# Kernel optimization log

Hardware: AMD Instinct MI355X
Metric: run time of the kernel (lower is better)

## Reference

```python
import jax, jax.numpy as jnp
import numpy as np

B, N = 2, 16384
GRID = (256, 256, 32)
LOWER = jnp.array([-51.2, -51.2, -3.2], jnp.float32)
UPPER = jnp.array([51.2, 51.2, 3.2], jnp.float32)
VOX = 0.4  # uniform voxel size (required by the SPC assertion in the original)
FREE = 17
MIN_DIST = 2.5
EVAL_LOWER = LOWER
EVAL_UPPER = UPPER
MAX_DIST = float(np.linalg.norm(np.array([102.4, 102.4, 6.4])))  # norm(upper - lower)
EPS = 1e-9


def setup_inputs() -> dict:
    key = jax.random.key(0)
    k_occ, k_sel, k_pts = jax.random.split(key, 3)
    labels = jax.random.randint(k_occ, (B,) + GRID, 0, 17, dtype=jnp.int32)
    sel = jax.random.uniform(k_sel, (B,) + GRID) < 0.05
    occupancy = jnp.where(sel, labels, FREE).astype(jnp.int32)
    # lidar points in sensor frame, xy in [-50, 50], z in [-3, 3]
    u = jax.random.uniform(k_pts, (B, N, 3), dtype=jnp.float32)
    points_lidar = u * jnp.array([100.0, 100.0, 6.0]) + jnp.array([-50.0, -50.0, -3.0])
    points_mask = jnp.ones((B, N), dtype=bool)
    T = jnp.eye(4, dtype=jnp.float32).at[:3, 3].set(jnp.array([0.8, 0.3, 1.7]))
    ego_from_lidar = jnp.broadcast_to(T, (B, 4, 4))
    return {
        "occupancy": occupancy,
        "points_lidar": points_lidar,
        "points_mask": points_mask,
        "ego_from_lidar": ego_from_lidar,
    }


def _apply_tf(T, p):
    # T: [B,4,4] homogeneous, p: [B,N,3]
    return jnp.einsum('bij,bnj->bni', T[:, :3, :3], p) + T[:, None, :3, 3]


def _traverse(occupancy, start_v, dirn, ray_len):
    """Exact voxel-grid ray traversal (replaces kaolin SPC unbatched_raytrace).

    start_v, dirn: [B,N,3] in voxel coordinates; ray_len: [B,N] in voxel units.
    Returns (first_hit_t [B,N] in voxel units, num_transmissions [B,N]).
    """
    Gx, Gy, Gz = GRID
    planes = jnp.concatenate([
        jnp.arange(Gx + 1), jnp.arange(Gy + 1), jnp.arange(Gz + 1)
    ]).astype(jnp.float32)  # [K]
    axid = jnp.concatenate([
        jnp.zeros(Gx + 1, jnp.int32), jnp.ones(Gy + 1, jnp.int32),
        jnp.full(Gz + 1, 2, jnp.int32)
    ])  # [K]
    s_ax = start_v[..., axid]          # [B,N,K]
    d_ax = dirn[..., axid]             # [B,N,K]
    t = jnp.where(jnp.abs(d_ax) > EPS, (planes - s_ax) / d_ax, jnp.inf)
    t = jnp.where(t >= 0.0, t, jnp.inf)          # only forward crossings
    b, n = start_v.shape[:2]
    t = jnp.concatenate([jnp.zeros((b, n, 1), t.dtype), t], axis=-1)  # start voxel at t=0
    t = jnp.sort(t, axis=-1)
    entry = t[..., :-1]
    tm = 0.5 * (entry + t[..., 1:])               # segment midpoints -> voxel ids
    vx = jnp.floor(start_v[..., 0][..., None] + tm * dirn[..., 0][..., None]).astype(jnp.int32)
    vy = jnp.floor(start_v[..., 1][..., None] + tm * dirn[..., 1][..., None]).astype(jnp.int32)
    vz = jnp.floor(start_v[..., 2][..., None] + tm * dirn[..., 2][..., None]).astype(jnp.int32)
    inb = ((vx >= 0) & (vx < Gx) & (vy >= 0) & (vy < Gy) & (vz >= 0) & (vz < Gz)
           & jnp.isfinite(tm))
    lin = (jnp.clip(vx, 0, Gx - 1) * Gy + jnp.clip(vy, 0, Gy - 1)) * Gz + jnp.clip(vz, 0, Gz - 1)
    occ_flat = occupancy.reshape(b, -1)
    k = lin.shape[-1]
    lbl = jax.vmap(jnp.take)(occ_flat, lin.reshape(b, -1)).reshape(b, n, k)
    occ_hit = inb & (lbl != FREE)
    first_t = jnp.min(jnp.where(occ_hit, entry, jnp.inf), axis=-1)
    ntrans = jnp.sum((occ_hit & (entry < ray_len[..., None])).astype(jnp.float32), axis=-1)
    return first_t, ntrans


def reference(occupancy, points_lidar, points_mask, ego_from_lidar):
    start_ego = jnp.broadcast_to(ego_from_lidar[:, None, :3, 3], points_lidar.shape)
    end_ego = _apply_tf(ego_from_lidar, points_lidar)
    # to voxel coordinates
    start_v = (start_ego - LOWER) / VOX
    end_v = (end_ego - LOWER) / VOX
    ray = end_v - start_v
    ray_len = jnp.linalg.norm(ray, axis=-1)
    dirn = ray / ray_len[..., None]
    first_t, ntrans = _traverse(occupancy, start_v, dirn, ray_len)
    depth = first_t * VOX  # back to metric units (scale)
    lidar_depth = jnp.linalg.norm(points_lidar, axis=-1)
    rendered = jnp.where(points_mask, depth, jnp.nan)
    ntrans = jnp.where(points_mask, ntrans, jnp.nan)
    finite_depth = jnp.isfinite(rendered) & points_mask & (lidar_depth > MIN_DIST)
    rendered = jnp.minimum(rendered, MAX_DIST)  # clamp_max (inf -> MAX_DIST)
    d_ego = end_ego - start_ego
    dn_ego = d_ego / jnp.linalg.norm(d_ego, axis=-1, keepdims=True)
    end_r = start_ego + dn_ego * rendered[..., None]
    # clamp_points_along_line into eval volume
    seg = end_r - start_ego
    t_ax = jnp.where(seg > 0, (EVAL_UPPER - start_ego) / seg,
                     jnp.where(seg < 0, (EVAL_LOWER - start_ego) / seg, jnp.inf))
    t_cl = jnp.clip(jnp.min(t_ax, axis=-1), 0.0, 1.0)
    end_c = start_ego + t_cl[..., None] * seg
    rendered = jnp.linalg.norm(end_c - start_ego, axis=-1)
    in_vol = (jnp.all(end_ego >= EVAL_LOWER, -1) & jnp.all(end_ego <= EVAL_UPPER, -1)
              & jnp.all(start_ego >= EVAL_LOWER, -1) & jnp.all(start_ego <= EVAL_UPPER, -1)
              & points_mask & (lidar_depth > MIN_DIST))
    return rendered, ntrans, lidar_depth, in_vol, finite_depth
```

## Files before the change

kernel.cpp:

```cpp
#include <hip/hip_runtime.h>
#include <math.h>

#define GXI 256
#define GYI 256
#define GZI 32
#define NVOX (GXI * GYI * GZI)
#define NWORDS (NVOX / 32)
#define KB 4
#define NSEG 16
#define LOG2SEG 4

__global__ __launch_bounds__(256) void build_bitmap_kernel(
    const int* __restrict__ occ, unsigned int* __restrict__ bits, int nvox_total)
{
    int v = blockIdx.x * blockDim.x + threadIdx.x;
    bool occupied = false;
    if (v < nvox_total) occupied = (occ[v] != 17);
    unsigned long long m = __ballot(occupied);
    if ((threadIdx.x & 63) == 0 && v < nvox_total) {
        *(unsigned long long*)&bits[v >> 5] = m;
    }
}

__global__ __launch_bounds__(256, 8) void render_lidar_kernel(
    const unsigned int* __restrict__ bits,
    const float* __restrict__ pts,
    const float* __restrict__ ego,
    float* __restrict__ out,
    int B, int N)
{
#pragma clang fp contract(off)
    const float LX = -51.2f, LY = -51.2f, LZ = -3.2f;
    const float UX =  51.2f, UY =  51.2f, UZ =  3.2f;
    const float VOX = 0.4f;
    const float EPS = 1e-9f;
    const float MIN_DIST = 2.5f;
    const float MAX_DIST = (float)144.95682129669906;
    const float INF = __builtin_inff();

    int tid = blockIdx.x * blockDim.x + threadIdx.x;
    int total = B * N;
    int idx = tid >> LOG2SEG;
    int seg = tid & (NSEG - 1);
    if (idx >= total) return;
    int b = idx / N;

    float svx, svy, svz, dx, dy, dz, ray_len;
    {
        const float* T = ego + (size_t)b * 16;
        float sx = T[3], sy = T[7], sz = T[11];
        const float* p = pts + (size_t)idx * 3;
        float px = p[0], py = p[1], pz = p[2];
        float ex = ((T[0]*px + T[1]*py) + T[2]*pz) + sx;
        float ey = ((T[4]*px + T[5]*py) + T[6]*pz) + sy;
        float ez = ((T[8]*px + T[9]*py) + T[10]*pz) + sz;

        svx = (sx - LX) / VOX; svy = (sy - LY) / VOX; svz = (sz - LZ) / VOX;
        float evx = (ex - LX) / VOX, evy = (ey - LY) / VOX, evz = (ez - LZ) / VOX;
        float rx = evx - svx, ry = evy - svy, rz = evz - svz;
        ray_len = sqrtf((rx*rx + ry*ry) + rz*rz);
        dx = rx / ray_len; dy = ry / ray_len; dz = rz / ray_len;
    }

    float s3[3] = {svx, svy, svz};
    float d3[3] = {dx, dy, dz};
    const float G3[3] = {(float)GXI, (float)GYI, (float)GZI};

    float t_exit = INF;
    #pragma unroll
    for (int a = 0; a < 3; ++a) {
        float da = d3[a];
        if (fabsf(da) > EPS) {
            float bound = (da > 0.0f) ? G3[a] : 0.0f;
            float te = (bound - s3[a]) / da;
            if (te < t_exit) t_exit = te;
        }
    }

    float lo = t_exit * ((float)seg / (float)NSEG);
    float hi = (seg == NSEG - 1) ? INF : t_exit * ((float)(seg + 1) / (float)NSEG);

    float taA[3], tbA[3], pnA[3];
    float t_pred = 0.0f;
    #pragma unroll
    for (int a = 0; a < 3; ++a) {
        float da = d3[a], s = s3[a], G = G3[a];
        if (fabsf(da) > EPS) {
            float g, st;
            if (seg == 0) {
                if (da > 0.0f) { g = ceilf(s);  if (g < 0.0f) g = 0.0f; st = 1.0f; }
                else           { g = floorf(s); if (g > G)    g = G;    st = -1.0f; }
            } else if (da > 0.0f) {
                g = ceilf(s + lo * da); if (g < 0.0f) g = 0.0f;
                int it = 0;
                while (it < 8 && g <= G && (g - s) / da <= lo) { g += 1.0f; ++it; }
                it = 0;
                while (it < 8 && g >= 1.0f && ((g - 1.0f) - s) / da > lo) { g -= 1.0f; ++it; }
                st = 1.0f;
                float pp = g - 1.0f;
                if (pp >= 0.0f && pp <= G) {
                    float c = (pp - s) / da;
                    if (c >= 0.0f && c > t_pred) t_pred = c;
                }
            } else {
                g = floorf(s + lo * da); if (g > G) g = G;
                int it = 0;
                while (it < 8 && g >= 0.0f && (g - s) / da <= lo) { g -= 1.0f; ++it; }
                it = 0;
                while (it < 8 && g + 1.0f <= G && ((g + 1.0f) - s) / da > lo) { g += 1.0f; ++it; }
                st = -1.0f;
                float pp = g + 1.0f;
                if (pp >= 0.0f && pp <= G) {
                    float c = (pp - s) / da;
                    if (c >= 0.0f && c > t_pred) t_pred = c;
                }
            }
            taA[a] = (g >= 0.0f && g <= G) ? (g - s) / da : INF;
            float p1 = g + st;
            tbA[a] = (p1 >= 0.0f && p1 <= G) ? (p1 - s) / da : INF;
            pnA[a] = p1 + st;
        } else {
            taA[a] = INF; tbA[a] = INF; pnA[a] = 0.0f;
        }
    }
    float ta0 = taA[0], ta1 = taA[1], ta2 = taA[2];
    float tb0 = tbA[0], tb1 = tbA[1], tb2 = tbA[2];
    float pn0 = pnA[0], pn1 = pnA[1], pn2 = pnA[2];

    const unsigned int* bm = bits + (size_t)b * NWORDS;
    float t_cur = t_pred;
    float first_t = INF;
    float ntrans = 0.0f;
    bool was_in = false, have_hit = false, done = false;
    int guard = 0;

    while (true) {
        float tent[KB];
        int   linv[KB];
        int   vmask = 0;

        #pragma unroll
        for (int k = 0; k < KB; ++k) {
            tent[k] = 0.0f; linv[k] = 0;
            if (done) continue;
            float tn = fminf(fminf(ta0, ta1), ta2);
            if (tn == INF || tn > hi) { done = true; continue; }

            float tm = 0.5f * (t_cur + tn);
            int ix = (int)floorf(svx + tm * dx);
            int iy = (int)floorf(svy + tm * dy);
            int iz = (int)floorf(svz + tm * dz);
            bool inb = ((unsigned)ix < 256u) && ((unsigned)iy < 256u)
                    && ((unsigned)iz < 32u);

            bool a0 = (ta0 == tn);
            bool a1 = !a0 && (ta1 == tn);
            bool a2 = !(a0 || a1);
            float np = a0 ? pn0 : (a1 ? pn1 : pn2);
            float ss = a0 ? svx : (a1 ? svy : svz);
            float dd = a0 ? dx  : (a1 ? dy  : dz);
            float GG = a2 ? 32.0f : 256.0f;
            float st = (dd > 0.0f) ? 1.0f : -1.0f;
            float tnew = (np >= 0.0f && np <= GG) ? (np - ss) / dd : INF;
            ta0 = a0 ? tb0 : ta0;  tb0 = a0 ? tnew : tb0;  pn0 = a0 ? pn0 + st : pn0;
            ta1 = a1 ? tb1 : ta1;  tb1 = a1 ? tnew : tb1;  pn1 = a1 ? pn1 + st : pn1;
            ta2 = a2 ? tb2 : ta2;  tb2 = a2 ? tnew : tb2;  pn2 = a2 ? pn2 + st : pn2;

            if (inb) {
                was_in = true;
                tent[k] = t_cur;
                linv[k] = (ix << 13) + (iy << 5) + iz;
                vmask |= (1 << k);
            } else if (was_in) {
                done = true;
            }
            t_cur = tn;
        }

        unsigned int w[KB];
        #pragma unroll
        for (int k = 0; k < KB; ++k) w[k] = bm[linv[k] >> 5];

        #pragma unroll
        for (int k = 0; k < KB; ++k) {
            if ((vmask >> k) & 1) {
                if ((w[k] >> (linv[k] & 31)) & 1u) {
                    if (!have_hit) { first_t = tent[k]; have_hit = true; }
                    if (tent[k] < ray_len) ntrans += 1.0f;
                }
            }
        }

        if (done || (have_hit && t_cur >= ray_len)) break;
        if (++guard > 256) break;
    }

    float ft = first_t;
    float nt = ntrans;
    #pragma unroll
    for (int off = 1; off < NSEG; off <<= 1) {
        float ofv = __shfl_xor(ft, off);
        float onv = __shfl_xor(nt, off);
        ft = fminf(ft, ofv);
        nt += onv;
    }
    if (seg != 0) return;
    have_hit = (ft < INF);

    const float* T = ego + (size_t)b * 16;
    float sx = T[3], sy = T[7], sz = T[11];
    const float* p = pts + (size_t)idx * 3;
    float px = p[0], py = p[1], pz = p[2];
    float ex = ((T[0]*px + T[1]*py) + T[2]*pz) + sx;
    float ey = ((T[4]*px + T[5]*py) + T[6]*pz) + sy;
    float ez = ((T[8]*px + T[9]*py) + T[10]*pz) + sz;

    float depth = ft * VOX;
    float lidar_depth = sqrtf((px*px + py*py) + pz*pz);
    bool finite_depth = have_hit && (lidar_depth > MIN_DIST);
    float rendered = fminf(depth, MAX_DIST);

    float dgx = ex - sx, dgy = ey - sy, dgz = ez - sz;
    float dgn = sqrtf((dgx*dgx + dgy*dgy) + dgz*dgz);
    float dnx = dgx / dgn, dny = dgy / dgn, dnz = dgz / dgn;
    float erx = sx + dnx * rendered;
    float ery = sy + dny * rendered;
    float erz = sz + dnz * rendered;
    float sgx = erx - sx, sgy = ery - sy, sgz = erz - sz;
    float tax = sgx > 0.0f ? (UX - sx) / sgx : (sgx < 0.0f ? (LX - sx) / sgx : INF);
    float tay = sgy > 0.0f ? (UY - sy) / sgy : (sgy < 0.0f ? (LY - sy) / sgy : INF);
    float taz = sgz > 0.0f ? (UZ - sz) / sgz : (sgz < 0.0f ? (LZ - sz) / sgz : INF);
    float tmin = fminf(fminf(tax, tay), taz);
    float tcl = fminf(fmaxf(tmin, 0.0f), 1.0f);
    float ecx = sx + tcl * sgx;
    float ecy = sy + tcl * sgy;
    float ecz = sz + tcl * sgz;
    float ocx = ecx - sx, ocy = ecy - sy, ocz = ecz - sz;
    float rout = sqrtf((ocx*ocx + ocy*ocy) + ocz*ocz);

    bool in_vol = (ex >= LX) && (ex <= UX) && (ey >= LY) && (ey <= UY)
               && (ez >= LZ) && (ez <= UZ)
               && (sx >= LX) && (sx <= UX) && (sy >= LY) && (sy <= UY)
               && (sz >= LZ) && (sz <= UZ)
               && (lidar_depth > MIN_DIST);

    out[idx]             = rout;
    out[total + idx]     = nt;
    out[2 * total + idx] = lidar_depth;
    out[3 * total + idx] = in_vol ? 1.0f : 0.0f;
    out[4 * total + idx] = finite_depth ? 1.0f : 0.0f;
}

extern "C" void kernel_launch(void* const* d_in, const int* in_sizes, int n_in,
                              void* d_out, int out_size, void* d_ws, size_t ws_size,
                              hipStream_t stream) {
    const int*   occ = (const int*)d_in[0];
    const float* pts = (const float*)d_in[1];
    const float* ego = (const float*)d_in[3];

    int BN = in_sizes[2];
    int B  = in_sizes[3] / 16;
    int N  = BN / B;

    unsigned int* bits = (unsigned int*)d_ws;
    int nvox_total = B * NVOX;

    int pthreads = 256;
    int pblocks  = (nvox_total + pthreads - 1) / pthreads;
    build_bitmap_kernel<<<pblocks, pthreads, 0, stream>>>(occ, bits, nvox_total);

    int threads = 256;
    long long tthreads = (long long)BN * NSEG;
    int blocks = (int)((tthreads + threads - 1) / threads);
    render_lidar_kernel<<<blocks, threads, 0, stream>>>(bits, pts, ego, (float*)d_out, B, N);
}
```

Baseline: 40.05 us.

## Split ray segments over the in-range span and add a fallback pass for misses

The 16 cooperating lanes now split only the traversal span up to min(ray_len, grid exit) instead of the whole grid-exit span. A lane stops once it passes ray_len even if no hit has been found yet. A second cooperative pass walks the span from ray_len to grid exit, but only when no lane found a hit, and it stops at the first occupied voxel. This is meant to spread the ntrans-counting work more evenly across lanes and avoid walking the full ray every time, at the cost of extra code, divergence and a possible second traversal on rays that miss.

```diff
diff --git a/kernel.cpp b/kernel.cpp
--- a/kernel.cpp
+++ b/kernel.cpp
@@ -19,6 +19,51 @@
     unsigned long long m = __ballot(occupied);
     if ((threadIdx.x & 63) == 0 && v < nvox_total) {
         *(unsigned long long*)&bits[v >> 5] = m;
+    }
+}
+
+__device__ __forceinline__ void axis_init(
+    float s, float da, float G, float lo, bool seg0,
+    float& ta, float& tb, float& pn, float& tpred)
+{
+    const float EPS = 1e-9f;
+    const float INF = __builtin_inff();
+    if (fabsf(da) > EPS) {
+        float g, st;
+        if (seg0) {
+            if (da > 0.0f) { g = ceilf(s);  if (g < 0.0f) g = 0.0f; st = 1.0f; }
+            else           { g = floorf(s); if (g > G)    g = G;    st = -1.0f; }
+        } else if (da > 0.0f) {
+            g = ceilf(s + lo * da); if (g < 0.0f) g = 0.0f;
+            int it = 0;
+            while (it < 8 && g <= G && (g - s) / da <= lo) { g += 1.0f; ++it; }
+            it = 0;
+            while (it < 8 && g >= 1.0f && ((g - 1.0f) - s) / da > lo) { g -= 1.0f; ++it; }
+            st = 1.0f;
+            float pp = g - 1.0f;
+            if (pp >= 0.0f && pp <= G) {
+                float c = (pp - s) / da;
+                if (c >= 0.0f && c > tpred) tpred = c;
+            }
+        } else {
+            g = floorf(s + lo * da); if (g > G) g = G;
+            int it = 0;
+            while (it < 8 && g >= 0.0f && (g - s) / da <= lo) { g -= 1.0f; ++it; }
+            it = 0;
+            while (it < 8 && g + 1.0f <= G && ((g + 1.0f) - s) / da > lo) { g += 1.0f; ++it; }
+            st = -1.0f;
+            float pp = g + 1.0f;
+            if (pp >= 0.0f && pp <= G) {
+                float c = (pp - s) / da;
+                if (c >= 0.0f && c > tpred) tpred = c;
+            }
+        }
+        ta = (g >= 0.0f && g <= G) ? (g - s) / da : INF;
+        float p1 = g + st;
+        tb = (p1 >= 0.0f && p1 <= G) ? (p1 - s) / da : INF;
+        pn = p1 + st;
+    } else {
+        ta = INF; tb = INF; pn = 0.0f;
     }
 }
 
@@ -62,70 +107,23 @@
         dx = rx / ray_len; dy = ry / ray_len; dz = rz / ray_len;
     }
 
-    float s3[3] = {svx, svy, svz};
-    float d3[3] = {dx, dy, dz};
-    const float G3[3] = {(float)GXI, (float)GYI, (float)GZI};
-
     float t_exit = INF;
-    #pragma unroll
-    for (int a = 0; a < 3; ++a) {
-        float da = d3[a];
-        if (fabsf(da) > EPS) {
-            float bound = (da > 0.0f) ? G3[a] : 0.0f;
-            float te = (bound - s3[a]) / da;
-            if (te < t_exit) t_exit = te;
-        }
-    }
-
-    float lo = t_exit * ((float)seg / (float)NSEG);
-    float hi = (seg == NSEG - 1) ? INF : t_exit * ((float)(seg + 1) / (float)NSEG);
-
-    float taA[3], tbA[3], pnA[3];
+    {
+        if (fabsf(dx) > EPS) { float te = ((dx > 0.0f ? 256.0f : 0.0f) - svx) / dx; if (te < t_exit) t_exit = te; }
+        if (fabsf(dy) > EPS) { float te = ((dy > 0.0f ? 256.0f : 0.0f) - svy) / dy; if (te < t_exit) t_exit = te; }
+        if (fabsf(dz) > EPS) { float te = ((dz > 0.0f ?  32.0f : 0.0f) - svz) / dz; if (te < t_exit) t_exit = te; }
+    }
+    float RLc = fminf(ray_len, t_exit);
+
+    float lo = RLc * ((float)seg / (float)NSEG);
+    float hi = (seg == NSEG - 1) ? INF : RLc * ((float)(seg + 1) / (float)NSEG);
+
+    float ta0, tb0, pn0, ta1, tb1, pn1, ta2, tb2, pn2;
     float t_pred = 0.0f;
-    #pragma unroll
-    for (int a = 0; a < 3; ++a) {
-        float da = d3[a], s = s3[a], G = G3[a];
-        if (fabsf(da) > EPS) {
-            float g, st;
-            if (seg == 0) {
-                if (da > 0.0f) { g = ceilf(s);  if (g < 0.0f) g = 0.0f; st = 1.0f; }
-                else           { g = floorf(s); if (g > G)    g = G;    st = -1.0f; }
-            } else if (da > 0.0f) {
-                g = ceilf(s + lo * da); if (g < 0.0f) g = 0.0f;
-                int it = 0;
-                while (it < 8 && g <= G && (g - s) / da <= lo) { g += 1.0f; ++it; }
-                it = 0;
-                while (it < 8 && g >= 1.0f && ((g - 1.0f) - s) / da > lo) { g -= 1.0f; ++it; }
-                st = 1.0f;
-                float pp = g - 1.0f;
-                if (pp >= 0.0f && pp <= G) {
-                    float c = (pp - s) / da;
-                    if (c >= 0.0f && c > t_pred) t_pred = c;
-                }
-            } else {
-                g = floorf(s + lo * da); if (g > G) g = G;
-                int it = 0;
-                while (it < 8 && g >= 0.0f && (g - s) / da <= lo) { g -= 1.0f; ++it; }
-                it = 0;
-                while (it < 8 && g + 1.0f <= G && ((g + 1.0f) - s) / da > lo) { g += 1.0f; ++it; }
-                st = -1.0f;
-                float pp = g + 1.0f;
-                if (pp >= 0.0f && pp <= G) {
-                    float c = (pp - s) / da;
-                    if (c >= 0.0f && c > t_pred) t_pred = c;
-                }
-            }
-            taA[a] = (g >= 0.0f && g <= G) ? (g - s) / da : INF;
-            float p1 = g + st;
-            tbA[a] = (p1 >= 0.0f && p1 <= G) ? (p1 - s) / da : INF;
-            pnA[a] = p1 + st;
-        } else {
-            taA[a] = INF; tbA[a] = INF; pnA[a] = 0.0f;
-        }
-    }
-    float ta0 = taA[0], ta1 = taA[1], ta2 = taA[2];
-    float tb0 = tbA[0], tb1 = tbA[1], tb2 = tbA[2];
-    float pn0 = pnA[0], pn1 = pnA[1], pn2 = pnA[2];
+    bool s0 = (seg == 0);
+    axis_init(svx, dx, 256.0f, lo, s0, ta0, tb0, pn0, t_pred);
+    axis_init(svy, dy, 256.0f, lo, s0, ta1, tb1, pn1, t_pred);
+    axis_init(svz, dz,  32.0f, lo, s0, ta2, tb2, pn2, t_pred);
 
     const unsigned int* bm = bits + (size_t)b * NWORDS;
     float t_cur = t_pred;
@@ -191,7 +189,7 @@
             }
         }
 
-        if (done || (have_hit && t_cur >= ray_len)) break;
+        if (done || t_cur >= ray_len) break;
         if (++guard > 256) break;
     }
 
@@ -204,6 +202,88 @@
         ft = fminf(ft, ofv);
         nt += onv;
     }
+
+    if (ft == INF && t_exit > ray_len) {
+        float span = t_exit - ray_len;
+        float lo2 = ray_len + span * ((float)seg / (float)NSEG);
+        float hi2 = (seg == NSEG - 1) ? INF
+                  : ray_len + span * ((float)(seg + 1) / (float)NSEG);
+        float tp2 = 0.0f;
+        axis_init(svx, dx, 256.0f, lo2, false, ta0, tb0, pn0, tp2);
+        axis_init(svy, dy, 256.0f, lo2, false, ta1, tb1, pn1, tp2);
+        axis_init(svz, dz,  32.0f, lo2, false, ta2, tb2, pn2, tp2);
+        t_cur = tp2; was_in = false; done = false;
+        float ft2 = INF; bool hit2 = false;
+        guard = 0;
+
+        while (true) {
+            float tent[KB];
+            int   linv[KB];
+            int   vmask = 0;
+
+            #pragma unroll
+            for (int k = 0; k < KB; ++k) {
+                tent[k] = 0.0f; linv[k] = 0;
+                if (done) continue;
+                float tn = fminf(fminf(ta0, ta1), ta2);
+                if (tn == INF || tn > hi2) { done = true; continue; }
+
+                float tm = 0.5f * (t_cur + tn);
+                int ix = (int)floorf(svx + tm * dx);
+                int iy = (int)floorf(svy + tm * dy);
+                int iz = (int)floorf(svz + tm * dz);
+                bool inb = ((unsigned)ix < 256u) && ((unsigned)iy < 256u)
+                        && ((unsigned)iz < 32u);
+
+                bool a0 = (ta0 == tn);
+                bool a1 = !a0 && (ta1 == tn);
+                bool a2 = !(a0 || a1);
+                float np = a0 ? pn0 : (a1 ? pn1 : pn2);
+                float ss = a0 ? svx : (a1 ? svy : svz);
+                float dd = a0 ? dx  : (a1 ? dy  : dz);
+                float GG = a2 ? 32.0f : 256.0f;
+                float st = (dd > 0.0f) ? 1.0f : -1.0f;
+                float tnew = (np >= 0.0f && np <= GG) ? (np - ss) / dd : INF;
+                ta0 = a0 ? tb0 : ta0;  tb0 = a0 ? tnew : tb0;  pn0 = a0 ? pn0 + st : pn0;
+                ta1 = a1 ? tb1 : ta1;  tb1 = a1 ? tnew : tb1;  pn1 = a1 ? pn1 + st : pn1;
+                ta2 = a2 ? tb2 : ta2;  tb2 = a2 ? tnew : tb2;  pn2 = a2 ? pn2 + st : pn2;
+
+                if (inb) {
+                    was_in = true;
+                    tent[k] = t_cur;
+                    linv[k] = (ix << 13) + (iy << 5) + iz;
+                    vmask |= (1 << k);
+                } else if (was_in) {
+                    done = true;
+                }
+                t_cur = tn;
+            }
+
+            unsigned int w[KB];
+            #pragma unroll
+            for (int k = 0; k < KB; ++k) w[k] = bm[linv[k] >> 5];
+
+            #pragma unroll
+            for (int k = 0; k < KB; ++k) {
+                if ((vmask >> k) & 1) {
+                    if (((w[k] >> (linv[k] & 31)) & 1u) && !hit2) {
+                        ft2 = tent[k]; hit2 = true;
+                    }
+                }
+            }
+
+            if (done || hit2) break;
+            if (++guard > 256) break;
+        }
+
+        #pragma unroll
+        for (int off = 1; off < NSEG; off <<= 1) {
+            float ofv = __shfl_xor(ft2, off);
+            ft2 = fminf(ft2, ofv);
+        }
+        ft = fminf(ft, ft2);
+    }
+
     if (seg != 0) return;
     have_hit = (ft < INF);
 
```

New measurement: 39.84 us. Within noise of the previous version (-0.5%).
